# Performance work log

Hardware: AMD Instinct MI355X
Metric: run time of the kernel (lower is better)

The kernel has to match this reference:

```python
import jax, jax.numpy as jnp
import numpy as np

B, N, D, L, NREPEAT = 32, 577, 384, 12, 4
H = 4 * D  # mlp hidden
EPS = 1e-6


def ln(x, w, b):
    mu = jnp.mean(x, axis=-1, keepdims=True)
    var = jnp.mean(jnp.square(x - mu), axis=-1, keepdims=True)
    return (x - mu) * jax.lax.rsqrt(var + EPS) * w + b


def setup_inputs() -> dict:
    key = jax.random.key(0)
    ks = jax.random.split(key, 16)
    s = 0.02
    return {
        "x": jax.random.normal(ks[0], (B, N, D), dtype=jnp.float32),
        "norm1_w": jnp.ones((L, D), jnp.float32),
        "norm1_b": jnp.zeros((L, D), jnp.float32),
        "qkv_w": jax.random.normal(ks[1], (L, 3 * D, D), jnp.float32) * s,
        "qkv_b": jnp.zeros((L, 3 * D), jnp.float32),
        "qn_w": jnp.ones((L, D), jnp.float32),
        "qn_b": jnp.zeros((L, D), jnp.float32),
        "kn_w": jnp.ones((L, D), jnp.float32),
        "kn_b": jnp.zeros((L, D), jnp.float32),
        "an_w": jnp.ones((L, D), jnp.float32),
        "an_b": jnp.zeros((L, D), jnp.float32),
        "proj_w": jax.random.normal(ks[2], (L, D, D), jnp.float32) * s,
        "proj_b": jnp.zeros((L, D), jnp.float32),
        "ls1": jnp.full((L, D), 1e-5, jnp.float32),
        "norm2_w": jnp.ones((L, D), jnp.float32),
        "norm2_b": jnp.zeros((L, D), jnp.float32),
        "fc1_w": jax.random.normal(ks[3], (L, H, D), jnp.float32) * s,
        "fc1_b": jnp.zeros((L, H), jnp.float32),
        "fc2_w": jax.random.normal(ks[4], (L, D, H), jnp.float32) * s,
        "fc2_b": jnp.zeros((L, D), jnp.float32),
        "ls2": jnp.full((L, D), 1e-5, jnp.float32),
    }


def _forward(x, norm1_w, norm1_b, qkv_w, qkv_b, qn_w, qn_b, kn_w, kn_b,
             an_w, an_b, proj_w, proj_b, ls1, norm2_w, norm2_b,
             fc1_w, fc1_b, fc2_w, fc2_b, ls2):
    scale = 1.0 / np.sqrt(D).astype(np.float32)
    x_prime = x
    history = []  # list of [B, 1, D] cls tokens, grows each repeat
    for _ in range(NREPEAT):
        new_cls = x[:, 0:1]
        x = jnp.concatenate([new_cls, x_prime[:, 1:]], axis=1)  # [B, N, D]
        mem = jnp.concatenate([x] + history, axis=1)            # [B, N+t, D]
        for l in range(L):
            res1 = x
            xn = ln(x, norm1_w[l], norm1_b[l])
            # manual qkv split: q from normed x, k/v from UNNORMED mem
            q = xn @ qkv_w[l, :D].T + qkv_b[l, :D]
            k = mem @ qkv_w[l, D:2 * D].T + qkv_b[l, D:2 * D]
            v = mem @ qkv_w[l, 2 * D:].T + qkv_b[l, 2 * D:]
            q = ln(q, qn_w[l], qn_b[l])
            k = ln(k, kn_w[l], kn_b[l])
            # single-head SDPA over full width D
            attn = jax.nn.softmax(jnp.einsum('bqd,bkd->bqk', q, k) * scale, axis=-1)
            prod = jnp.einsum('bqk,bkd->bqd', attn, v)
            prod = ln(prod, an_w[l], an_b[l])
            proj = prod @ proj_w[l].T + proj_b[l]
            x = proj * ls1[l] + res1
            res2 = x
            x2 = ln(x, norm2_w[l], norm2_b[l])
            h = jax.nn.gelu(x2 @ fc1_w[l].T + fc1_b[l], approximate=False)
            x1 = h @ fc2_w[l].T + fc2_b[l]
            x = x1 * ls2[l] + res2
        history.append(new_cls)
    return x


def reference(x, norm1_w, norm1_b, qkv_w, qkv_b, qn_w, qn_b, kn_w, kn_b,
              an_w, an_b, proj_w, proj_b, ls1, norm2_w, norm2_b,
              fc1_w, fc1_b, fc2_w, fc2_b, ls2):
    return _forward(x, norm1_w, norm1_b, qkv_w, qkv_b, qn_w, qn_b, kn_w, kn_b,
                    an_w, an_b, proj_w, proj_b, ls1, norm2_w, norm2_b,
                    fc1_w, fc1_b, fc2_w, fc2_b, ls2)
```

## Files before the change

### kernel.cpp

```cpp
#include <hip/hip_runtime.h>
#include <math.h>

#define BB 32
#define NN 577
#define DD 384
#define HD 1536
#define LL 12
#define MP 640
#define NRPT 4

typedef __attribute__((ext_vector_type(8))) short bf16x8;
typedef __attribute__((ext_vector_type(4))) float f32x4;

__device__ __forceinline__ unsigned short f2bf(float f){
  unsigned u = __builtin_bit_cast(unsigned, f);
  u += 0x7fffu + ((u >> 16) & 1u);
  return (unsigned short)(u >> 16);
}
__device__ __forceinline__ float bf2f(unsigned short s){
  unsigned u = ((unsigned)s) << 16;
  return __builtin_bit_cast(float, u);
}

__device__ __forceinline__ void async16(void* lds, const void* g){
  __builtin_amdgcn_global_load_lds(
      (const __attribute__((address_space(1))) unsigned int*)g,
      (__attribute__((address_space(3))) unsigned int*)lds, 16, 0, 0);
}

__global__ void prep_k(float* __restrict__ x, const float* __restrict__ xp,
                       float* __restrict__ cls_r, const float* __restrict__ cls_hist,
                       unsigned short* __restrict__ mem, int r){
  int i = blockIdx.x * 256 + threadIdx.x;
  if (i >= BB*MP*DD) return;
  int d = i % DD;
  int n = (i / DD) % MP;
  int b = i / (MP*DD);
  float v; bool wr = true;
  if (n == 0){ v = x[(size_t)b*NN*DD + d]; cls_r[b*DD + d] = v; }
  else if (n < NN){ v = xp[((size_t)b*NN + n)*DD + d]; x[((size_t)b*NN + n)*DD + d] = v; wr = (r==0); }
  else if (n < NN + r){ v = cls_hist[(size_t)(n-NN)*BB*DD + b*DD + d]; wr = (n == NN + r - 1); }
  else { v = 0.f; wr = (r==0); }
  if (wr) mem[i] = f2bf(v);
}

__global__ void cast_all_k(const float* __restrict__ qkvw, const float* __restrict__ pw,
                           const float* __restrict__ f1w, const float* __restrict__ f2w,
                           unsigned short* __restrict__ wbuf){
  int i = blockIdx.x * 256 + threadIdx.x;
  const int QKV = 3*DD*DD;
  const int PRJ = DD*DD;
  const int F1  = HD*DD;
  const int TOT = QKV + PRJ + 2*F1;
  if (i >= LL*TOT) return;
  int l = i / TOT, j = i % TOT;
  float v;
  if (j < QKV) v = qkvw[(size_t)l*QKV + j];
  else if (j < QKV+PRJ) v = pw[(size_t)l*PRJ + (j-QKV)];
  else if (j < QKV+PRJ+F1) v = f1w[(size_t)l*F1 + (j-QKV-PRJ)];
  else v = f2w[(size_t)l*F1 + (j-QKV-PRJ-F1)];
  wbuf[i] = f2bf(v);
}

template<typename T>
__global__ __launch_bounds__(256) void ln4_k(const T* __restrict__ in, const float* __restrict__ w,
                                             const float* __restrict__ bias, unsigned short* __restrict__ out,
                                             int nrows){
  int row = blockIdx.x*4 + (threadIdx.x >> 6);
  if (row >= nrows) return;
  int lane = threadIdx.x & 63;
  const T* p = in + (size_t)row*DD;
  float v[6];
  if constexpr (sizeof(T) == 4){
    const float* pf = (const float*)p;
    float4 a = *(const float4*)(pf + lane*4);
    float2 c = *(const float2*)(pf + 256 + lane*2);
    v[0]=a.x; v[1]=a.y; v[2]=a.z; v[3]=a.w; v[4]=c.x; v[5]=c.y;
  } else {
    const unsigned short* ps = (const unsigned short*)p;
    ushort4 a = *(const ushort4*)(ps + lane*4);
    ushort2 c = *(const ushort2*)(ps + 256 + lane*2);
    v[0]=bf2f(a.x); v[1]=bf2f(a.y); v[2]=bf2f(a.z); v[3]=bf2f(a.w);
    v[4]=bf2f(c.x); v[5]=bf2f(c.y);
  }
  float s = v[0]+v[1]+v[2]+v[3]+v[4]+v[5];
  #pragma unroll
  for (int o=32;o;o>>=1) s += __shfl_xor(s, o, 64);
  float mu = s * (1.f/DD);
  float q = 0.f;
  #pragma unroll
  for (int i=0;i<6;i++){ float t = v[i]-mu; q += t*t; }
  #pragma unroll
  for (int o=32;o;o>>=1) q += __shfl_xor(q, o, 64);
  float rs = rsqrtf(q*(1.f/DD) + 1e-6f);
  float4 w4 = *(const float4*)(w + lane*4);
  float2 w2 = *(const float2*)(w + 256 + lane*2);
  float4 b4 = *(const float4*)(bias + lane*4);
  float2 b2 = *(const float2*)(bias + 256 + lane*2);
  unsigned short* po = out + (size_t)row*DD;
  ushort4 o4;
  o4.x = f2bf((v[0]-mu)*rs*w4.x + b4.x);
  o4.y = f2bf((v[1]-mu)*rs*w4.y + b4.y);
  o4.z = f2bf((v[2]-mu)*rs*w4.z + b4.z);
  o4.w = f2bf((v[3]-mu)*rs*w4.w + b4.w);
  *(ushort4*)(po + lane*4) = o4;
  ushort2 o2;
  o2.x = f2bf((v[4]-mu)*rs*w2.x + b2.x);
  o2.y = f2bf((v[5]-mu)*rs*w2.y + b2.y);
  *(ushort2*)(po + 256 + lane*2) = o2;
}

__global__ __launch_bounds__(256) void fixup_k(
    const unsigned short* __restrict__ mem,
    const unsigned short* __restrict__ wq,
    const float* __restrict__ qkvb,
    const float* __restrict__ knw, const float* __restrict__ knb,
    unsigned short* __restrict__ kc,
    unsigned short* __restrict__ vc,
    int row2){
  int task = blockIdx.x*4 + (threadIdx.x >> 6);
  int lane = threadIdx.x & 63;
  int kind = task & 1;
  int rsel = (task >> 1) & 1;
  int b    = task >> 2;
  int row  = rsel ? row2 : 0;
  const unsigned short* mrow = mem + ((size_t)b*MP + row)*DD;
  const unsigned short* W = wq + (size_t)(kind+1)*DD*DD;
  const float* bias = qkvb + (kind+1)*DD;

  float acc[6] = {0,0,0,0,0,0};
  for (int i=0;i<48;i++){
    bf16x8 m8 = *(const bf16x8*)(mrow + i*8);
    float mf[8];
    #pragma unroll
    for (int j=0;j<8;j++) mf[j] = bf2f((unsigned short)m8[j]);
    #pragma unroll
    for (int c=0;c<6;c++){
      bf16x8 w8 = *(const bf16x8*)(W + (size_t)(lane + c*64)*DD + i*8);
      #pragma unroll
      for (int j=0;j<8;j++) acc[c] += mf[j]*bf2f((unsigned short)w8[j]);
    }
  }
  #pragma unroll
  for (int c=0;c<6;c++) acc[c] += bias[lane + c*64];

  if (kind == 0){
    float s1 = 0.f, s2 = 0.f;
    #pragma unroll
    for (int c=0;c<6;c++){ s1 += acc[c]; s2 += acc[c]*acc[c]; }
    #pragma unroll
    for (int o=32;o;o>>=1){ s1 += __shfl_xor(s1, o, 64); s2 += __shfl_xor(s2, o, 64); }
    float mu = s1*(1.f/DD);
    float var = s2*(1.f/DD) - mu*mu;
    float rs = rsqrtf(fmaxf(var, 0.f) + 1e-6f);
    unsigned short* out = kc + ((size_t)b*MP + row)*DD;
    #pragma unroll
    for (int c=0;c<6;c++){
      int col = lane + c*64;
      out[col] = f2bf((acc[c]-mu)*rs*knw[col] + knb[col]);
    }
  } else {
    #pragma unroll
    for (int c=0;c<6;c++){
      int d = lane + c*64;
      vc[((size_t)b*DD + d)*MP + row] = f2bf(acc[c]);
    }
  }
}

__device__ __forceinline__ void gemm_body(
    unsigned short (*a_sh)[128*32], unsigned short (*b_sh)[128*32],
    const unsigned short* __restrict__ Ab, int lda, int arows,
    const unsigned short* __restrict__ Bb, int ldb, int brows,
    const float* __restrict__ bias, int K, int N,
    unsigned short* __restrict__ oB, int ldo, int orows,
    int epi, int row0, int col0){

  int tid  = threadIdx.x;
  int wave = tid >> 6, lane = tid & 63;
  int lr = lane & 15, kg = lane >> 4;
  int wm = wave >> 1, wn = wave & 1;

  f32x4 zf = {0.f,0.f,0.f,0.f};
  f32x4 acc[4][4];
  #pragma unroll
  for (int i=0;i<4;i++)
    #pragma unroll
    for (int j=0;j<4;j++) acc[i][j] = zf;

  int ra[2], rb[2], kc[2];
  #pragma unroll
  for (int it=0; it<2; it++){
    int c = tid + it*256;
    int r = row0 + (c>>2); if (r > arows-1) r = arows-1;
    ra[it] = r;
    r = col0 + (c>>2); if (r > brows-1) r = brows-1;
    rb[it] = r;
    kc[it] = (c&3)*8;
  }

  for (int k0 = 0; k0 < K; k0 += 64){
    #pragma unroll
    for (int p=0;p<2;p++){
      #pragma unroll
      for (int it=0; it<2; it++){
        async16(&a_sh[p][(it*256 + wave*64)*8], Ab + (size_t)ra[it]*lda + k0 + p*32 + kc[it]);
        async16(&b_sh[p][(it*256 + wave*64)*8], Bb + (size_t)rb[it]*ldb + k0 + p*32 + kc[it]);
      }
    }
    __syncthreads();
    #pragma unroll
    for (int p=0;p<2;p++){
      bf16x8 af[4], bfr[4];
      #pragma unroll
      for (int i=0;i<4;i++){
        af[i]  = *(const bf16x8*)&a_sh[p][(wm*64 + i*16 + lr)*32 + kg*8];
        bfr[i] = *(const bf16x8*)&b_sh[p][(wn*64 + i*16 + lr)*32 + kg*8];
      }
      #pragma unroll
      for (int i=0;i<4;i++)
        #pragma unroll
        for (int j=0;j<4;j++)
          acc[i][j] = __builtin_amdgcn_mfma_f32_16x16x32_bf16(af[i], bfr[j], acc[i][j], 0,0,0);
    }
    __syncthreads();
  }

  #pragma unroll
  for (int mi=0;mi<4;mi++)
    #pragma unroll
    for (int ni=0;ni<4;ni++)
      #pragma unroll
      for (int r=0;r<4;r++){
        int row = row0 + wm*64 + mi*16 + kg*4 + r;
        int col = col0 + wn*64 + ni*16 + lr;
        if (row >= orows || col >= N) continue;
        float vv = acc[mi][ni][r];
        vv += (epi == 0) ? bias[col] : bias[row];
        oB[(size_t)row*ldo + col] = f2bf(vv);
      }
}

__global__ __launch_bounds__(256) void gemmqkv_k(
    const unsigned short* __restrict__ xn, const unsigned short* __restrict__ mem,
    const unsigned short* __restrict__ wq, const float* __restrict__ qkvb,
    unsigned short* __restrict__ qout, unsigned short* __restrict__ kout,
    unsigned short* __restrict__ vout, int QR){

  __shared__ unsigned short a_sh[2][128*32];
  __shared__ unsigned short b_sh[2][128*32];

  int bid = blockIdx.x;
  const unsigned short *A, *B;
  const float* bias;
  unsigned short* out;
  int arows, brows, N, ldo, orows, epi, row0, col0;

  if (bid < 435){
    int gx = bid % 3, gy = bid / 3;
    A = xn; arows = QR; B = wq; brows = 384;
    bias = qkvb; N = 384; out = qout; ldo = 384; orows = QR; epi = 0;
    row0 = gy*128; col0 = gx*128;
  } else if (bid < 915){
    int t = bid - 435; int gx = t % 3, gy = t / 3;
    A = mem; arows = BB*MP; B = wq + DD*DD; brows = 384;
    bias = qkvb + DD; N = 384; out = kout; ldo = 384; orows = BB*MP; epi = 0;
    row0 = gy*128; col0 = gx*128;
  } else {
    int t = bid - 915; int z = t/15; int rem = t%15; int gx = rem % 5, gy = rem / 5;
    A = wq + 2*DD*DD; arows = 384;
    B = mem + (size_t)z*MP*DD; brows = MP;
    bias = qkvb + 2*DD; N = MP; out = vout + (size_t)z*DD*MP; ldo = MP; orows = 384; epi = 1;
    row0 = gy*128; col0 = gx*128;
  }
  gemm_body(a_sh, b_sh, A, 384, arows, B, 384, brows, bias, 384, N, out, ldo, orows, epi, row0, col0);
}

template<int EPI>
__global__ __launch_bounds__(256) void gemm128(
    const unsigned short* __restrict__ A, int lda, int arows, long sA,
    const unsigned short* __restrict__ B, int ldb, int brows, long sB,
    const float* __restrict__ bias,
    int K, int N,
    float* __restrict__ outF, unsigned short* __restrict__ outB,
    int ldo, int orows, long sO,
    const float* __restrict__ ls){

  __shared__ unsigned short a_sh[2][128*32];
  __shared__ unsigned short b_sh[2][128*32];

  int tid  = threadIdx.x;
  int wave = tid >> 6, lane = tid & 63;
  int lr = lane & 15, kg = lane >> 4;
  int wm = wave >> 1, wn = wave & 1;
  int z = blockIdx.z;
  int row0 = blockIdx.y * 128;
  int col0 = blockIdx.x * 128;

  const unsigned short* Ab = A + (size_t)z*sA;
  const unsigned short* Bb = B + (size_t)z*sB;

  f32x4 zf = {0.f,0.f,0.f,0.f};
  f32x4 acc[4][4];
  #pragma unroll
  for (int i=0;i<4;i++)
    #pragma unroll
    for (int j=0;j<4;j++) acc[i][j] = zf;

  int ra[2], rb[2], kc[2];
  #pragma unroll
  for (int it=0; it<2; it++){
    int c = tid + it*256;
    int r = row0 + (c>>2); if (r > arows-1) r = arows-1;
    ra[it] = r;
    r = col0 + (c>>2); if (r > brows-1) r = brows-1;
    rb[it] = r;
    kc[it] = (c&3)*8;
  }

  for (int k0 = 0; k0 < K; k0 += 64){
    #pragma unroll
    for (int p=0;p<2;p++){
      #pragma unroll
      for (int it=0; it<2; it++){
        unsigned short* la = &a_sh[p][(it*256 + wave*64)*8];
        unsigned short* lb = &b_sh[p][(it*256 + wave*64)*8];
        async16(la, Ab + (size_t)ra[it]*lda + k0 + p*32 + kc[it]);
        async16(lb, Bb + (size_t)rb[it]*ldb + k0 + p*32 + kc[it]);
      }
    }
    __syncthreads();
    #pragma unroll
    for (int p=0;p<2;p++){
      bf16x8 af[4], bfr[4];
      #pragma unroll
      for (int i=0;i<4;i++){
        af[i]  = *(const bf16x8*)&a_sh[p][(wm*64 + i*16 + lr)*32 + kg*8];
        bfr[i] = *(const bf16x8*)&b_sh[p][(wn*64 + i*16 + lr)*32 + kg*8];
      }
      #pragma unroll
      for (int i=0;i<4;i++)
        #pragma unroll
        for (int j=0;j<4;j++)
          acc[i][j] = __builtin_amdgcn_mfma_f32_16x16x32_bf16(af[i], bfr[j], acc[i][j], 0,0,0);
    }
    __syncthreads();
  }

  float* oF = outF ? outF + (size_t)z*sO : nullptr;
  unsigned short* oB = outB ? outB + (size_t)z*sO : nullptr;

  #pragma unroll
  for (int mi=0;mi<4;mi++)
    #pragma unroll
    for (int ni=0;ni<4;ni++)
      #pragma unroll
      for (int r=0;r<4;r++){
        int row = row0 + wm*64 + mi*16 + kg*4 + r;
        int col = col0 + wn*64 + ni*16 + lr;
        if (row >= orows || col >= N) continue;
        float vv = acc[mi][ni][r];
        size_t idx = (size_t)row*ldo + col;
        if (EPI == 0){
          if (bias) vv += bias[col];
          oB[idx] = f2bf(vv);
        } else if (EPI == 1){
          vv += bias[row];
          oB[idx] = f2bf(vv);
        } else if (EPI == 2){
          vv += bias[col];
          oF[idx] = vv*ls[col] + oF[idx];
        } else {
          vv += bias[col];
          float g = 0.5f*vv*(1.f + erff(vv*0.70710678118f));
          oB[idx] = f2bf(g);
        }
      }
}

__global__ __launch_bounds__(256, 2) void attn_k(
    const unsigned short* __restrict__ qraw,
    const float* __restrict__ qw, const float* __restrict__ qb_,
    const unsigned short* __restrict__ kb,
    const unsigned short* __restrict__ vT,
    const float* __restrict__ anw, const float* __restrict__ anb,
    unsigned short* __restrict__ out, int M){

  __shared__ unsigned short k_sh[32*384];
  __shared__ unsigned short v_sh[384*32];
  __shared__ unsigned short p_sh[64*56];

  int tid = threadIdx.x;
  int wv = tid >> 6, lane = tid & 63;
  int lr = lane & 15, kg = lane >> 4;
  int b = blockIdx.y, qt0 = blockIdx.x * 64;

  bf16x8 qf[12];
  {
    int qrow = qt0 + wv*16 + lr; if (qrow > NN-1) qrow = NN-1;
    const unsigned short* qp = qraw + ((size_t)b*NN + qrow)*DD;
    float s1 = 0.f, s2 = 0.f;
    #pragma unroll
    for (int ks=0; ks<12; ks++){
      qf[ks] = *(const bf16x8*)(qp + ks*32 + kg*8);
      #pragma unroll
      for (int j=0;j<8;j++){
        float t = bf2f((unsigned short)qf[ks][j]);
        s1 += t; s2 += t*t;
      }
    }
    s1 += __shfl_xor(s1, 16, 64); s1 += __shfl_xor(s1, 32, 64);
    s2 += __shfl_xor(s2, 16, 64); s2 += __shfl_xor(s2, 32, 64);
    const float SC = 0.05103103588f;
    float mu = s1 * (1.f/DD);
    float var = s2 * (1.f/DD) - mu*mu;
    float rs = rsqrtf(fmaxf(var, 0.f) + 1e-6f) * SC;
    #pragma unroll
    for (int ks=0; ks<12; ks++){
      int c0 = ks*32 + kg*8;
      float4 wa = *(const float4*)(qw + c0);
      float4 wb = *(const float4*)(qw + c0 + 4);
      float4 ba = *(const float4*)(qb_ + c0);
      float4 bb = *(const float4*)(qb_ + c0 + 4);
      bf16x8 t;
      t[0] = (short)f2bf((bf2f((unsigned short)qf[ks][0])-mu)*rs*wa.x + ba.x*SC);
      t[1] = (short)f2bf((bf2f((unsigned short)qf[ks][1])-mu)*rs*wa.y + ba.y*SC);
      t[2] = (short)f2bf((bf2f((unsigned short)qf[ks][2])-mu)*rs*wa.z + ba.z*SC);
      t[3] = (short)f2bf((bf2f((unsigned short)qf[ks][3])-mu)*rs*wa.w + ba.w*SC);
      t[4] = (short)f2bf((bf2f((unsigned short)qf[ks][4])-mu)*rs*wb.x + bb.x*SC);
      t[5] = (short)f2bf((bf2f((unsigned short)qf[ks][5])-mu)*rs*wb.y + bb.y*SC);
      t[6] = (short)f2bf((bf2f((unsigned short)qf[ks][6])-mu)*rs*wb.z + bb.z*SC);
      t[7] = (short)f2bf((bf2f((unsigned short)qf[ks][7])-mu)*rs*wb.w + bb.w*SC);
      qf[ks] = t;
    }
  }

  f32x4 zf = {0.f,0.f,0.f,0.f};
  f32x4 O[24];
  #pragma unroll
  for (int i=0;i<24;i++) O[i] = zf;
  float m_run[4], l_run[4];
  #pragma unroll
  for (int r=0;r<4;r++){ m_run[r] = -INFINITY; l_run[r] = 0.f; }

  for (int kt=0; kt<19; kt++){
    __syncthreads();
    #pragma unroll
    for (int i=0;i<6;i++){
      int L = i*256 + tid;
      int row = L/48, c = L%48;
      int gc = (c & ~7) | ((c ^ row) & 7);
      async16(&k_sh[L*8], kb + ((size_t)b*MP + kt*32 + row)*DD + gc*8);
    }
    #pragma unroll
    for (int i=0;i<6;i++){
      int L = i*256 + tid;
      int row = L>>2;
      int gc = (L&3) ^ (row&3);
      async16(&v_sh[L*8], vT + ((size_t)b*DD + row)*MP + kt*32 + gc*8);
    }
    __syncthreads();

    f32x4 s[2] = {zf, zf};
    __builtin_amdgcn_s_setprio(1);
    #pragma unroll
    for (int ks=0; ks<12; ks++){
      int c = ks*4 + kg;
      #pragma unroll
      for (int nk=0; nk<2; nk++){
        int krow = nk*16 + lr;
        bf16x8 bk = *(const bf16x8*)&k_sh[krow*DD + ((c & ~7) | ((c ^ krow)&7))*8];
        s[nk] = __builtin_amdgcn_mfma_f32_16x16x32_bf16(qf[ks], bk, s[nk], 0,0,0);
      }
    }
    __builtin_amdgcn_s_setprio(0);
    #pragma unroll
    for (int nk=0; nk<2; nk++){
      if (kt*32 + nk*16 + lr >= M){
        s[nk][0] = -INFINITY; s[nk][1] = -INFINITY; s[nk][2] = -INFINITY; s[nk][3] = -INFINITY;
      }
    }
    float vmax[4];
    #pragma unroll
    for (int r=0;r<4;r++){
      float v = fmaxf(s[0][r], s[1][r]);
      v = fmaxf(v, __shfl_xor(v, 1, 64));
      v = fmaxf(v, __shfl_xor(v, 2, 64));
      v = fmaxf(v, __shfl_xor(v, 4, 64));
      v = fmaxf(v, __shfl_xor(v, 8, 64));
      vmax[r] = v;
    }
    bool small = (vmax[0] <= m_run[0] + 8.f) & (vmax[1] <= m_run[1] + 8.f)
               & (vmax[2] <= m_run[2] + 8.f) & (vmax[3] <= m_run[3] + 8.f);
    if (!__all(small)){
      #pragma unroll
      for (int r=0;r<4;r++){
        float mn = fmaxf(m_run[r], vmax[r]);
        float al = __expf(m_run[r] - mn);
        m_run[r] = mn;
        l_run[r] *= al;
        #pragma unroll
        for (int ni=0;ni<24;ni++) O[ni][r] *= al;
      }
    }
    #pragma unroll
    for (int nk=0;nk<2;nk++)
      #pragma unroll
      for (int r=0;r<4;r++)
        s[nk][r] = __expf(s[nk][r] - m_run[r]);
    #pragma unroll
    for (int r=0;r<4;r++){
      float v = s[0][r] + s[1][r];
      v += __shfl_xor(v, 1, 64);
      v += __shfl_xor(v, 2, 64);
      v += __shfl_xor(v, 4, 64);
      v += __shfl_xor(v, 8, 64);
      l_run[r] += v;
    }
    #pragma unroll
    for (int nk=0;nk<2;nk++)
      #pragma unroll
      for (int r=0;r<4;r++)
        p_sh[(wv*16 + kg*4 + r)*56 + nk*16 + lr] = f2bf(s[nk][r]);
    __syncthreads();

    bf16x8 ap = *(const bf16x8*)&p_sh[(wv*16 + lr)*56 + kg*8];
    __builtin_amdgcn_s_setprio(1);
    #pragma unroll
    for (int ni=0;ni<24;ni++){
      int d = ni*16 + lr;
      bf16x8 bv = *(const bf16x8*)&v_sh[d*32 + ((kg ^ (d&3))*8)];
      O[ni] = __builtin_amdgcn_mfma_f32_16x16x32_bf16(ap, bv, O[ni], 0,0,0);
    }
    __builtin_amdgcn_s_setprio(0);
  }

  float inv[4];
  #pragma unroll
  for (int r=0;r<4;r++) inv[r] = 1.f / l_run[r];
  float s1[4] = {0,0,0,0}, s2[4] = {0,0,0,0};
  #pragma unroll
  for (int ni=0;ni<24;ni++)
    #pragma unroll
    for (int r=0;r<4;r++){
      float x = O[ni][r]*inv[r];
      O[ni][r] = x;
      s1[r] += x; s2[r] += x*x;
    }
  #pragma unroll
  for (int r=0;r<4;r++){
    #pragma unroll
    for (int o=1;o<16;o<<=1){ s1[r] += __shfl_xor(s1[r], o, 64); s2[r] += __shfl_xor(s2[r], o, 64); }
  }
  float mu[4], rs[4];
  #pragma unroll
  for (int r=0;r<4;r++){
    mu[r] = s1[r]*(1.f/DD);
    float var = s2[r]*(1.f/DD) - mu[r]*mu[r];
    rs[r] = rsqrtf(fmaxf(var, 0.f) + 1e-6f);
  }
  int rowb = qt0 + wv*16 + kg*4;
  #pragma unroll
  for (int ni=0;ni<24;ni++){
    int col = ni*16 + lr;
    float wc = anw[col], bc = anb[col];
    #pragma unroll
    for (int r=0;r<4;r++){
      int qrow = rowb + r;
      if (qrow < NN)
        out[((size_t)b*NN + qrow)*DD + col] = f2bf((O[ni][r]-mu[r])*rs[r]*wc + bc);
    }
  }
}


extern "C" void kernel_launch(void* const* d_in, const int* in_sizes, int n_in,
                              void* d_out, int out_size, void* d_ws, size_t ws_size,
                              hipStream_t stream){
  const float* x_in = (const float*)d_in[0];
  const float* n1w  = (const float*)d_in[1];
  const float* n1b  = (const float*)d_in[2];
  const float* qkvw = (const float*)d_in[3];
  const float* qkvb = (const float*)d_in[4];
  const float* qnw  = (const float*)d_in[5];
  const float* qnb  = (const float*)d_in[6];
  const float* knw  = (const float*)d_in[7];
  const float* knb  = (const float*)d_in[8];
  const float* anw  = (const float*)d_in[9];
  const float* anb  = (const float*)d_in[10];
  const float* pw   = (const float*)d_in[11];
  const float* pb   = (const float*)d_in[12];
  const float* ls1  = (const float*)d_in[13];
  const float* n2w  = (const float*)d_in[14];
  const float* n2b  = (const float*)d_in[15];
  const float* f1w  = (const float*)d_in[16];
  const float* f1b  = (const float*)d_in[17];
  const float* f2w  = (const float*)d_in[18];
  const float* f2bb = (const float*)d_in[19];
  const float* ls2  = (const float*)d_in[20];

  char* ws = (char*)d_ws;
  size_t off = 0;
  auto alloc = [&](size_t bytes)->char* {
    char* p = ws + off;
    off = (off + bytes + 255) & ~(size_t)255;
    return p;
  };

  const int QKV = 3*DD*DD, PRJ = DD*DD, F1 = HD*DD;
  const size_t WTOT = (size_t)QKV + PRJ + 2*F1;
  const size_t SLOT = (size_t)BB*MP*DD;

  unsigned short* wbuf  = (unsigned short*)alloc((size_t)LL*WTOT*2);
  float*          cls_h = (float*)         alloc((size_t)NRPT*BB*DD*4);
  unsigned short* mem_bf= (unsigned short*)alloc(SLOT*2);
  unsigned short* pool  = (unsigned short*)alloc(6*SLOT*2);
  unsigned short* kcache = (unsigned short*)alloc((size_t)LL*SLOT*2);
  unsigned short* vcache = (unsigned short*)alloc((size_t)LL*SLOT*2);
  bool use_cache = (off <= ws_size);

  unsigned short* S0 = pool;
  unsigned short* S1 = pool + SLOT;
  unsigned short* S2 = pool + 2*SLOT;
  unsigned short* S3 = pool + 3*SLOT;
  unsigned short* S5 = pool + 5*SLOT;

  unsigned short* xn    = S0;
  unsigned short* qraw  = S1;
  unsigned short* prodn = S3;
  unsigned short* x2    = S0;
  unsigned short* h     = S1;

  float* xf = (float*)d_out;

  auto cg = [](size_t n){ return dim3((unsigned)((n + 255) / 256)); };

  hipMemcpyAsync(xf, x_in, (size_t)BB*NN*DD*4, hipMemcpyDeviceToDevice, stream);

  const int RT  = (BB*NN + 127)/128;
  const int QR  = BB*NN;
  const int KR  = BB*MP;

  cast_all_k<<<cg((size_t)LL*WTOT),256,0,stream>>>(qkvw, pw, f1w, f2w, wbuf);

  for (int r = 0; r < NRPT; r++){
    int M = NN + r;
    prep_k<<<cg((size_t)BB*MP*DD),256,0,stream>>>(xf, x_in, cls_h + (size_t)r*BB*DD, cls_h, mem_bf, r);
    for (int l = 0; l < LL; l++){
      const unsigned short* wl = wbuf + (size_t)l*WTOT;
      const unsigned short* wq = wl;
      const unsigned short* wp = wl + QKV;
      const unsigned short* w1 = wl + QKV + PRJ;
      const unsigned short* w2 = wl + QKV + PRJ + F1;

      bool cached = use_cache;
      unsigned short* kbuf = cached ? kcache + (size_t)l*SLOT : S2;
      unsigned short* vbuf = cached ? vcache + (size_t)l*SLOT : S5;

      ln4_k<float><<<cg((size_t)QR*64),256,0,stream>>>(xf, n1w + l*DD, n1b + l*DD, xn, QR);

      if (!cached || r == 0){
        gemmqkv_k<<<1395,256,0,stream>>>(xn, mem_bf, wq, qkvb + l*3*DD, qraw, kbuf, vbuf, QR);
        ln4_k<unsigned short><<<cg((size_t)KR*64),256,0,stream>>>(kbuf, knw + l*DD, knb + l*DD, kbuf, KR);
      } else {
        gemm128<0><<<dim3(3,RT,1),256,0,stream>>>(xn,384,QR,0, wq,384,384,0,
            qkvb + l*3*DD, 384,384, nullptr,qraw,384,QR,0, nullptr);
        fixup_k<<<32,256,0,stream>>>(mem_bf, wq, qkvb + l*3*DD,
                                     knw + l*DD, knb + l*DD, kbuf, vbuf, NN + r - 1);
      }

      attn_k<<<dim3(10,BB),256,0,stream>>>(qraw, qnw + l*DD, qnb + l*DD, kbuf, vbuf,
                                           anw + l*DD, anb + l*DD, prodn, M);
      gemm128<2><<<dim3(3,RT,1),256,0,stream>>>(prodn,384,QR,0, wp,384,384,0,
          pb + l*DD, 384,384, xf,nullptr,384,QR,0, ls1 + l*DD);
      ln4_k<float><<<cg((size_t)QR*64),256,0,stream>>>(xf, n2w + l*DD, n2b + l*DD, x2, QR);
      gemm128<3><<<dim3(HD/128,RT,1),256,0,stream>>>(x2,384,QR,0, w1,384,HD,0,
          f1b + l*HD, 384,HD, nullptr,h,HD,QR,0, nullptr);
      gemm128<2><<<dim3(3,RT,1),256,0,stream>>>(h,HD,QR,0, w2,HD,384,0,
          f2bb + l*DD, HD,384, xf,nullptr,384,QR,0, ls2 + l*DD);
    }
  }
}
```

Baseline: 15.62 ms.

## Batch K/V projection and K-norm across all layers into single launches

```diff
diff --git a/kernel.cpp b/kernel.cpp
--- a/kernel.cpp
+++ b/kernel.cpp
@@ -110,23 +110,68 @@
   *(ushort2*)(po + 256 + lane*2) = o2;
 }
 
-__global__ __launch_bounds__(256) void fixup_k(
+__global__ __launch_bounds__(256) void kln_all_k(
+    unsigned short* __restrict__ kbase, long kstride,
+    const float* __restrict__ knw, const float* __restrict__ knb, int l0){
+  const int RPL4 = (BB*MP)/4;
+  int li = blockIdx.x / RPL4;
+  int row = (blockIdx.x % RPL4)*4 + (threadIdx.x >> 6);
+  int lane = threadIdx.x & 63;
+  unsigned short* p = kbase + (size_t)li*kstride + (size_t)row*DD;
+  const float* w = knw + (size_t)(l0+li)*DD;
+  const float* bias = knb + (size_t)(l0+li)*DD;
+  float v[6];
+  ushort4 a = *(const ushort4*)(p + lane*4);
+  ushort2 c = *(const ushort2*)(p + 256 + lane*2);
+  v[0]=bf2f(a.x); v[1]=bf2f(a.y); v[2]=bf2f(a.z); v[3]=bf2f(a.w);
+  v[4]=bf2f(c.x); v[5]=bf2f(c.y);
+  float s = v[0]+v[1]+v[2]+v[3]+v[4]+v[5];
+  #pragma unroll
+  for (int o=32;o;o>>=1) s += __shfl_xor(s, o, 64);
+  float mu = s * (1.f/DD);
+  float q = 0.f;
+  #pragma unroll
+  for (int i=0;i<6;i++){ float t = v[i]-mu; q += t*t; }
+  #pragma unroll
+  for (int o=32;o;o>>=1) q += __shfl_xor(q, o, 64);
+  float rs = rsqrtf(q*(1.f/DD) + 1e-6f);
+  float4 w4 = *(const float4*)(w + lane*4);
+  float2 w2 = *(const float2*)(w + 256 + lane*2);
+  float4 b4 = *(const float4*)(bias + lane*4);
+  float2 b2 = *(const float2*)(bias + 256 + lane*2);
+  ushort4 o4;
+  o4.x = f2bf((v[0]-mu)*rs*w4.x + b4.x);
+  o4.y = f2bf((v[1]-mu)*rs*w4.y + b4.y);
+  o4.z = f2bf((v[2]-mu)*rs*w4.z + b4.z);
+  o4.w = f2bf((v[3]-mu)*rs*w4.w + b4.w);
+  *(ushort4*)(p + lane*4) = o4;
+  ushort2 o2;
+  o2.x = f2bf((v[4]-mu)*rs*w2.x + b2.x);
+  o2.y = f2bf((v[5]-mu)*rs*w2.y + b2.y);
+  *(ushort2*)(p + 256 + lane*2) = o2;
+}
+
+__global__ __launch_bounds__(256) void fixup_all_k(
     const unsigned short* __restrict__ mem,
-    const unsigned short* __restrict__ wq,
+    const unsigned short* __restrict__ wbuf,
     const float* __restrict__ qkvb,
-    const float* __restrict__ knw, const float* __restrict__ knb,
-    unsigned short* __restrict__ kc,
-    unsigned short* __restrict__ vc,
+    const float* __restrict__ knw_, const float* __restrict__ knb_,
+    unsigned short* __restrict__ kcache,
+    unsigned short* __restrict__ vcache,
     int row2){
-  int task = blockIdx.x*4 + (threadIdx.x >> 6);
+  const int QKV = 3*DD*DD, PRJ = DD*DD, F1 = HD*DD;
+  const size_t WTOT = (size_t)QKV + PRJ + 2*F1;
+  const size_t SLOT = (size_t)BB*MP*DD;
+  int l    = blockIdx.x >> 5;
+  int task = (blockIdx.x & 31)*4 + (threadIdx.x >> 6);
   int lane = threadIdx.x & 63;
   int kind = task & 1;
   int rsel = (task >> 1) & 1;
   int b    = task >> 2;
   int row  = rsel ? row2 : 0;
   const unsigned short* mrow = mem + ((size_t)b*MP + row)*DD;
-  const unsigned short* W = wq + (size_t)(kind+1)*DD*DD;
-  const float* bias = qkvb + (kind+1)*DD;
+  const unsigned short* W = wbuf + (size_t)l*WTOT + (size_t)(kind+1)*DD*DD;
+  const float* bias = qkvb + (size_t)l*3*DD + (kind+1)*DD;
 
   float acc[6] = {0,0,0,0,0,0};
   for (int i=0;i<48;i++){
@@ -153,13 +198,16 @@
     float mu = s1*(1.f/DD);
     float var = s2*(1.f/DD) - mu*mu;
     float rs = rsqrtf(fmaxf(var, 0.f) + 1e-6f);
-    unsigned short* out = kc + ((size_t)b*MP + row)*DD;
+    const float* knw = knw_ + (size_t)l*DD;
+    const float* knb = knb_ + (size_t)l*DD;
+    unsigned short* out = kcache + (size_t)l*SLOT + ((size_t)b*MP + row)*DD;
     #pragma unroll
     for (int c=0;c<6;c++){
       int col = lane + c*64;
       out[col] = f2bf((acc[c]-mu)*rs*knw[col] + knb[col]);
     }
   } else {
+    unsigned short* vc = vcache + (size_t)l*SLOT;
     #pragma unroll
     for (int c=0;c<6;c++){
       int d = lane + c*64;
@@ -241,6 +289,35 @@
       }
 }
 
+__global__ __launch_bounds__(256) void kv_mega_k(
+    const unsigned short* __restrict__ mem,
+    const unsigned short* __restrict__ wbuf,
+    const float* __restrict__ qkvb,
+    unsigned short* __restrict__ kbase, long kstride,
+    unsigned short* __restrict__ vbase, long vstride,
+    int l0){
+  __shared__ unsigned short a_sh[2][128*32];
+  __shared__ unsigned short b_sh[2][128*32];
+  const int QKV = 3*DD*DD, PRJ = DD*DD, F1 = HD*DD;
+  const size_t WTOT = (size_t)QKV + PRJ + 2*F1;
+
+  int li = blockIdx.x / 960;
+  int t  = blockIdx.x % 960;
+  int l  = l0 + li;
+  const unsigned short* wl = wbuf + (size_t)l*WTOT;
+  const float* bl = qkvb + (size_t)l*3*DD;
+
+  if (t < 480){
+    int gx = t % 3, gy = t / 3;
+    gemm_body(a_sh, b_sh, mem, 384, BB*MP, wl + DD*DD, 384, 384, bl + DD,
+              384, 384, kbase + (size_t)li*kstride, 384, BB*MP, 0, gy*128, gx*128);
+  } else {
+    int u = t - 480; int z = u/15; int rem = u%15; int gx = rem % 5, gy = rem / 5;
+    gemm_body(a_sh, b_sh, wl + 2*DD*DD, 384, 384, mem + (size_t)z*MP*DD, 384, MP, bl + 2*DD,
+              384, MP, vbase + (size_t)li*vstride + (size_t)z*DD*MP, MP, 384, 1, gy*128, gx*128);
+  }
+}
+
 __global__ __launch_bounds__(256) void gemmqkv_k(
     const unsigned short* __restrict__ xn, const unsigned short* __restrict__ mem,
     const unsigned short* __restrict__ wq, const float* __restrict__ qkvb,
@@ -251,29 +328,19 @@
   __shared__ unsigned short b_sh[2][128*32];
 
   int bid = blockIdx.x;
-  const unsigned short *A, *B;
-  const float* bias;
-  unsigned short* out;
-  int arows, brows, N, ldo, orows, epi, row0, col0;
-
   if (bid < 435){
     int gx = bid % 3, gy = bid / 3;
-    A = xn; arows = QR; B = wq; brows = 384;
-    bias = qkvb; N = 384; out = qout; ldo = 384; orows = QR; epi = 0;
-    row0 = gy*128; col0 = gx*128;
+    gemm_body(a_sh, b_sh, xn, 384, QR, wq, 384, 384, qkvb, 384, 384,
+              qout, 384, QR, 0, gy*128, gx*128);
   } else if (bid < 915){
     int t = bid - 435; int gx = t % 3, gy = t / 3;
-    A = mem; arows = BB*MP; B = wq + DD*DD; brows = 384;
-    bias = qkvb + DD; N = 384; out = kout; ldo = 384; orows = BB*MP; epi = 0;
-    row0 = gy*128; col0 = gx*128;
+    gemm_body(a_sh, b_sh, mem, 384, BB*MP, wq + DD*DD, 384, 384, qkvb + DD,
+              384, 384, kout, 384, BB*MP, 0, gy*128, gx*128);
   } else {
     int t = bid - 915; int z = t/15; int rem = t%15; int gx = rem % 5, gy = rem / 5;
-    A = wq + 2*DD*DD; arows = 384;
-    B = mem + (size_t)z*MP*DD; brows = MP;
-    bias = qkvb + 2*DD; N = MP; out = vout + (size_t)z*DD*MP; ldo = MP; orows = 384; epi = 1;
-    row0 = gy*128; col0 = gx*128;
-  }
-  gemm_body(a_sh, b_sh, A, 384, arows, B, 384, brows, bias, 384, N, out, ldo, orows, epi, row0, col0);
+    gemm_body(a_sh, b_sh, wq + 2*DD*DD, 384, 384, mem + (size_t)z*MP*DD, 384, MP, qkvb + 2*DD,
+              384, MP, vout + (size_t)z*DD*MP, MP, 384, 1, gy*128, gx*128);
+  }
 }
 
 template<int EPI>
@@ -599,37 +666,50 @@
   const float* f2bb = (const float*)d_in[19];
   const float* ls2  = (const float*)d_in[20];
 
+  const int QKV = 3*DD*DD, PRJ = DD*DD, F1 = HD*DD;
+  const size_t WTOT = (size_t)QKV + PRJ + 2*F1;
+  const size_t SLOT = (size_t)BB*MP*DD;
+  const size_t SLB  = SLOT*2;
+
   char* ws = (char*)d_ws;
   size_t off = 0;
-  auto alloc = [&](size_t bytes)->char* {
+  auto take = [&](size_t bytes)->char* {
     char* p = ws + off;
     off = (off + bytes + 255) & ~(size_t)255;
     return p;
   };
 
-  const int QKV = 3*DD*DD, PRJ = DD*DD, F1 = HD*DD;
-  const size_t WTOT = (size_t)QKV + PRJ + 2*F1;
-  const size_t SLOT = (size_t)BB*MP*DD;
-
-  unsigned short* wbuf  = (unsigned short*)alloc((size_t)LL*WTOT*2);
-  float*          cls_h = (float*)         alloc((size_t)NRPT*BB*DD*4);
-  unsigned short* mem_bf= (unsigned short*)alloc(SLOT*2);
-  unsigned short* pool  = (unsigned short*)alloc(6*SLOT*2);
-  unsigned short* kcache = (unsigned short*)alloc((size_t)LL*SLOT*2);
-  unsigned short* vcache = (unsigned short*)alloc((size_t)LL*SLOT*2);
-  bool use_cache = (off <= ws_size);
-
-  unsigned short* S0 = pool;
-  unsigned short* S1 = pool + SLOT;
-  unsigned short* S2 = pool + 2*SLOT;
-  unsigned short* S3 = pool + 3*SLOT;
-  unsigned short* S5 = pool + 5*SLOT;
+  unsigned short* wbuf   = (unsigned short*)take((size_t)LL*WTOT*2);
+  float*          cls_h  = (float*)         take((size_t)NRPT*BB*DD*4);
+  unsigned short* mem_bf = (unsigned short*)take(SLB);
+  unsigned short* S0     = (unsigned short*)take(SLB);
+  unsigned short* S3     = (unsigned short*)take(SLB);
+  unsigned short* HQ     = (unsigned short*)take(4*SLB);
+
+  bool fullcache = (off + 2*(size_t)LL*SLB <= ws_size);
+  int G = 0;
+  unsigned short *kvk = nullptr, *kvv = nullptr;
+  long kstr = 0, vstr = 0;
+  if (fullcache){
+    kvk = (unsigned short*)take((size_t)LL*SLB);
+    kvv = (unsigned short*)take((size_t)LL*SLB);
+    kstr = (long)SLOT; vstr = (long)SLOT;
+    G = LL;
+  } else {
+    size_t avail = (ws_size > off) ? ws_size - off : 0;
+    G = (int)(avail / (2*SLB)); if (G > LL) G = LL; if (G < 0) G = 0;
+    if (G > 0){
+      kvk = (unsigned short*)take((size_t)G*2*SLB);
+      kvv = kvk + SLOT;
+      kstr = (long)(2*SLOT); vstr = (long)(2*SLOT);
+    }
+  }
 
   unsigned short* xn    = S0;
-  unsigned short* qraw  = S1;
+  unsigned short* x2    = S0;
   unsigned short* prodn = S3;
-  unsigned short* x2    = S0;
-  unsigned short* h     = S1;
+  unsigned short* qraw  = HQ;
+  unsigned short* h     = HQ;
 
   float* xf = (float*)d_out;
 
@@ -646,29 +726,16 @@
   for (int r = 0; r < NRPT; r++){
     int M = NN + r;
     prep_k<<<cg((size_t)BB*MP*DD),256,0,stream>>>(xf, x_in, cls_h + (size_t)r*BB*DD, cls_h, mem_bf, r);
-    for (int l = 0; l < LL; l++){
+
+    auto chain7 = [&](int l, unsigned short* kbuf, unsigned short* vbuf){
       const unsigned short* wl = wbuf + (size_t)l*WTOT;
       const unsigned short* wq = wl;
       const unsigned short* wp = wl + QKV;
       const unsigned short* w1 = wl + QKV + PRJ;
       const unsigned short* w2 = wl + QKV + PRJ + F1;
-
-      bool cached = use_cache;
-      unsigned short* kbuf = cached ? kcache + (size_t)l*SLOT : S2;
-      unsigned short* vbuf = cached ? vcache + (size_t)l*SLOT : S5;
-
       ln4_k<float><<<cg((size_t)QR*64),256,0,stream>>>(xf, n1w + l*DD, n1b + l*DD, xn, QR);
-
-      if (!cached || r == 0){
-        gemmqkv_k<<<1395,256,0,stream>>>(xn, mem_bf, wq, qkvb + l*3*DD, qraw, kbuf, vbuf, QR);
-        ln4_k<unsigned short><<<cg((size_t)KR*64),256,0,stream>>>(kbuf, knw + l*DD, knb + l*DD, kbuf, KR);
-      } else {
-        gemm128<0><<<dim3(3,RT,1),256,0,stream>>>(xn,384,QR,0, wq,384,384,0,
-            qkvb + l*3*DD, 384,384, nullptr,qraw,384,QR,0, nullptr);
-        fixup_k<<<32,256,0,stream>>>(mem_bf, wq, qkvb + l*3*DD,
-                                     knw + l*DD, knb + l*DD, kbuf, vbuf, NN + r - 1);
-      }
-
+      gemm128<0><<<dim3(3,RT,1),256,0,stream>>>(xn,384,QR,0, wq,384,384,0,
+          qkvb + l*3*DD, 384,384, nullptr,qraw,384,QR,0, nullptr);
       attn_k<<<dim3(10,BB),256,0,stream>>>(qraw, qnw + l*DD, qnb + l*DD, kbuf, vbuf,
                                            anw + l*DD, anb + l*DD, prodn, M);
       gemm128<2><<<dim3(3,RT,1),256,0,stream>>>(prodn,384,QR,0, wp,384,384,0,
@@ -678,6 +745,47 @@
           f1b + l*HD, 384,HD, nullptr,h,HD,QR,0, nullptr);
       gemm128<2><<<dim3(3,RT,1),256,0,stream>>>(h,HD,QR,0, w2,HD,384,0,
           f2bb + l*DD, HD,384, xf,nullptr,384,QR,0, ls2 + l*DD);
-    }
-  }
-}
+    };
+
+    if (fullcache){
+      if (r == 0){
+        kv_mega_k<<<LL*960,256,0,stream>>>(mem_bf, wbuf, qkvb, kvk, kstr, kvv, vstr, 0);
+        kln_all_k<<<LL*(KR/4),256,0,stream>>>(kvk, kstr, knw, knb, 0);
+      } else {
+        fixup_all_k<<<LL*32,256,0,stream>>>(mem_bf, wbuf, qkvb, knw, knb, kvk, kvv, NN + r - 1);
+      }
+      for (int l = 0; l < LL; l++)
+        chain7(l, kvk + (size_t)l*kstr, kvv + (size_t)l*vstr);
+    } else if (G > 0){
+      for (int g0 = 0; g0 < LL; g0 += G){
+        int gc = (g0 + G <= LL) ? G : (LL - g0);
+        kv_mega_k<<<gc*960,256,0,stream>>>(mem_bf, wbuf, qkvb, kvk, kstr, kvv, vstr, g0);
+        kln_all_k<<<gc*(KR/4),256,0,stream>>>(kvk, kstr, knw, knb, g0);
+        for (int l = g0; l < g0 + gc; l++)
+          chain7(l, kvk + (size_t)(l-g0)*kstr, kvv + (size_t)(l-g0)*vstr);
+      }
+    } else {
+      for (int l = 0; l < LL; l++){
+        const unsigned short* wl = wbuf + (size_t)l*WTOT;
+        const unsigned short* wq = wl;
+        const unsigned short* wp = wl + QKV;
+        const unsigned short* w1 = wl + QKV + PRJ;
+        const unsigned short* w2 = wl + QKV + PRJ + F1;
+        unsigned short* kbuf = S3;
+        unsigned short* vbuf = HQ + 2*SLOT;
+        ln4_k<float><<<cg((size_t)QR*64),256,0,stream>>>(xf, n1w + l*DD, n1b + l*DD, xn, QR);
+        gemmqkv_k<<<1395,256,0,stream>>>(xn, mem_bf, wq, qkvb + l*3*DD, qraw, kbuf, vbuf, QR);
+        kln_all_k<<<(KR/4),256,0,stream>>>(kbuf, 0, knw + l*DD, knb + l*DD, 0);
+        attn_k<<<dim3(10,BB),256,0,stream>>>(qraw, qnw + l*DD, qnb + l*DD, kbuf, vbuf,
+                                             anw + l*DD, anb + l*DD, prodn, M);
+        gemm128<2><<<dim3(3,RT,1),256,0,stream>>>(prodn,384,QR,0, wp,384,384,0,
+            pb + l*DD, 384,384, xf,nullptr,384,QR,0, ls1 + l*DD);
+        ln4_k<float><<<cg((size_t)QR*64),256,0,stream>>>(xf, n2w + l*DD, n2b + l*DD, x2, QR);
+        gemm128<3><<<dim3(HD/128,RT,1),256,0,stream>>>(x2,384,QR,0, w1,384,HD,0,
+            f1b + l*HD, 384,HD, nullptr,h,HD,QR,0, nullptr);
+        gemm128<2><<<dim3(3,RT,1),256,0,stream>>>(h,HD,QR,0, w2,HD,384,0,
+            f2bb + l*DD, HD,384, xf,nullptr,384,QR,0, ls2 + l*DD);
+      }
+    }
+  }
+}
```

New measurement: 15.66 ms. About the same (+0.3%).

## Drop cross-repeat K/V cache and fuse key LayerNorm into attention tile loads

Applied to the files above, without the earlier changes.

```diff
diff --git a/kernel.cpp b/kernel.cpp
--- a/kernel.cpp
+++ b/kernel.cpp
@@ -62,27 +62,17 @@
   wbuf[i] = f2bf(v);
 }
 
-template<typename T>
-__global__ __launch_bounds__(256) void ln4_k(const T* __restrict__ in, const float* __restrict__ w,
+__global__ __launch_bounds__(256) void ln4_k(const float* __restrict__ in, const float* __restrict__ w,
                                              const float* __restrict__ bias, unsigned short* __restrict__ out,
                                              int nrows){
   int row = blockIdx.x*4 + (threadIdx.x >> 6);
   if (row >= nrows) return;
   int lane = threadIdx.x & 63;
-  const T* p = in + (size_t)row*DD;
+  const float* pf = in + (size_t)row*DD;
   float v[6];
-  if constexpr (sizeof(T) == 4){
-    const float* pf = (const float*)p;
-    float4 a = *(const float4*)(pf + lane*4);
-    float2 c = *(const float2*)(pf + 256 + lane*2);
-    v[0]=a.x; v[1]=a.y; v[2]=a.z; v[3]=a.w; v[4]=c.x; v[5]=c.y;
-  } else {
-    const unsigned short* ps = (const unsigned short*)p;
-    ushort4 a = *(const ushort4*)(ps + lane*4);
-    ushort2 c = *(const ushort2*)(ps + 256 + lane*2);
-    v[0]=bf2f(a.x); v[1]=bf2f(a.y); v[2]=bf2f(a.z); v[3]=bf2f(a.w);
-    v[4]=bf2f(c.x); v[5]=bf2f(c.y);
-  }
+  float4 a = *(const float4*)(pf + lane*4);
+  float2 c = *(const float2*)(pf + 256 + lane*2);
+  v[0]=a.x; v[1]=a.y; v[2]=a.z; v[3]=a.w; v[4]=c.x; v[5]=c.y;
   float s = v[0]+v[1]+v[2]+v[3]+v[4]+v[5];
   #pragma unroll
   for (int o=32;o;o>>=1) s += __shfl_xor(s, o, 64);
@@ -110,64 +100,6 @@
   *(ushort2*)(po + 256 + lane*2) = o2;
 }
 
-__global__ __launch_bounds__(256) void fixup_k(
-    const unsigned short* __restrict__ mem,
-    const unsigned short* __restrict__ wq,
-    const float* __restrict__ qkvb,
-    const float* __restrict__ knw, const float* __restrict__ knb,
-    unsigned short* __restrict__ kc,
-    unsigned short* __restrict__ vc,
-    int row2){
-  int task = blockIdx.x*4 + (threadIdx.x >> 6);
-  int lane = threadIdx.x & 63;
-  int kind = task & 1;
-  int rsel = (task >> 1) & 1;
-  int b    = task >> 2;
-  int row  = rsel ? row2 : 0;
-  const unsigned short* mrow = mem + ((size_t)b*MP + row)*DD;
-  const unsigned short* W = wq + (size_t)(kind+1)*DD*DD;
-  const float* bias = qkvb + (kind+1)*DD;
-
-  float acc[6] = {0,0,0,0,0,0};
-  for (int i=0;i<48;i++){
-    bf16x8 m8 = *(const bf16x8*)(mrow + i*8);
-    float mf[8];
-    #pragma unroll
-    for (int j=0;j<8;j++) mf[j] = bf2f((unsigned short)m8[j]);
-    #pragma unroll
-    for (int c=0;c<6;c++){
-      bf16x8 w8 = *(const bf16x8*)(W + (size_t)(lane + c*64)*DD + i*8);
-      #pragma unroll
-      for (int j=0;j<8;j++) acc[c] += mf[j]*bf2f((unsigned short)w8[j]);
-    }
-  }
-  #pragma unroll
-  for (int c=0;c<6;c++) acc[c] += bias[lane + c*64];
-
-  if (kind == 0){
-    float s1 = 0.f, s2 = 0.f;
-    #pragma unroll
-    for (int c=0;c<6;c++){ s1 += acc[c]; s2 += acc[c]*acc[c]; }
-    #pragma unroll
-    for (int o=32;o;o>>=1){ s1 += __shfl_xor(s1, o, 64); s2 += __shfl_xor(s2, o, 64); }
-    float mu = s1*(1.f/DD);
-    float var = s2*(1.f/DD) - mu*mu;
-    float rs = rsqrtf(fmaxf(var, 0.f) + 1e-6f);
-    unsigned short* out = kc + ((size_t)b*MP + row)*DD;
-    #pragma unroll
-    for (int c=0;c<6;c++){
-      int col = lane + c*64;
-      out[col] = f2bf((acc[c]-mu)*rs*knw[col] + knb[col]);
-    }
-  } else {
-    #pragma unroll
-    for (int c=0;c<6;c++){
-      int d = lane + c*64;
-      vc[((size_t)b*DD + d)*MP + row] = f2bf(acc[c]);
-    }
-  }
-}
-
 __device__ __forceinline__ void gemm_body(
     unsigned short (*a_sh)[128*32], unsigned short (*b_sh)[128*32],
     const unsigned short* __restrict__ Ab, int lda, int arows,
@@ -251,29 +183,19 @@
   __shared__ unsigned short b_sh[2][128*32];
 
   int bid = blockIdx.x;
-  const unsigned short *A, *B;
-  const float* bias;
-  unsigned short* out;
-  int arows, brows, N, ldo, orows, epi, row0, col0;
-
   if (bid < 435){
     int gx = bid % 3, gy = bid / 3;
-    A = xn; arows = QR; B = wq; brows = 384;
-    bias = qkvb; N = 384; out = qout; ldo = 384; orows = QR; epi = 0;
-    row0 = gy*128; col0 = gx*128;
+    gemm_body(a_sh, b_sh, xn, 384, QR, wq, 384, 384, qkvb, 384, 384,
+              qout, 384, QR, 0, gy*128, gx*128);
   } else if (bid < 915){
     int t = bid - 435; int gx = t % 3, gy = t / 3;
-    A = mem; arows = BB*MP; B = wq + DD*DD; brows = 384;
-    bias = qkvb + DD; N = 384; out = kout; ldo = 384; orows = BB*MP; epi = 0;
-    row0 = gy*128; col0 = gx*128;
+    gemm_body(a_sh, b_sh, mem, 384, BB*MP, wq + DD*DD, 384, 384, qkvb + DD,
+              384, 384, kout, 384, BB*MP, 0, gy*128, gx*128);
   } else {
     int t = bid - 915; int z = t/15; int rem = t%15; int gx = rem % 5, gy = rem / 5;
-    A = wq + 2*DD*DD; arows = 384;
-    B = mem + (size_t)z*MP*DD; brows = MP;
-    bias = qkvb + 2*DD; N = MP; out = vout + (size_t)z*DD*MP; ldo = MP; orows = 384; epi = 1;
-    row0 = gy*128; col0 = gx*128;
-  }
-  gemm_body(a_sh, b_sh, A, 384, arows, B, 384, brows, bias, 384, N, out, ldo, orows, epi, row0, col0);
+    gemm_body(a_sh, b_sh, wq + 2*DD*DD, 384, 384, mem + (size_t)z*MP*DD, 384, MP, qkvb + 2*DD,
+              384, MP, vout + (size_t)z*DD*MP, MP, 384, 1, gy*128, gx*128);
+  }
 }
 
 template<int EPI>
@@ -361,13 +283,7 @@
         if (row >= orows || col >= N) continue;
         float vv = acc[mi][ni][r];
         size_t idx = (size_t)row*ldo + col;
-        if (EPI == 0){
-          if (bias) vv += bias[col];
-          oB[idx] = f2bf(vv);
-        } else if (EPI == 1){
-          vv += bias[row];
-          oB[idx] = f2bf(vv);
-        } else if (EPI == 2){
+        if (EPI == 2){
           vv += bias[col];
           oF[idx] = vv*ls[col] + oF[idx];
         } else {
@@ -381,7 +297,8 @@
 __global__ __launch_bounds__(256, 2) void attn_k(
     const unsigned short* __restrict__ qraw,
     const float* __restrict__ qw, const float* __restrict__ qb_,
-    const unsigned short* __restrict__ kb,
+    const unsigned short* __restrict__ kraw,
+    const float* __restrict__ knw, const float* __restrict__ knb,
     const unsigned short* __restrict__ vT,
     const float* __restrict__ anw, const float* __restrict__ anb,
     unsigned short* __restrict__ out, int M){
@@ -450,7 +367,7 @@
       int L = i*256 + tid;
       int row = L/48, c = L%48;
       int gc = (c & ~7) | ((c ^ row) & 7);
-      async16(&k_sh[L*8], kb + ((size_t)b*MP + kt*32 + row)*DD + gc*8);
+      async16(&k_sh[L*8], kraw + ((size_t)b*MP + kt*32 + row)*DD + gc*8);
     }
     #pragma unroll
     for (int i=0;i<6;i++){
@@ -458,6 +375,45 @@
       int row = L>>2;
       int gc = (L&3) ^ (row&3);
       async16(&v_sh[L*8], vT + ((size_t)b*DD + row)*MP + kt*32 + gc*8);
+    }
+    __syncthreads();
+
+    {
+      int row8 = tid >> 3;
+      int sub  = tid & 7;
+      unsigned short* kr = &k_sh[row8*384];
+      float s1 = 0.f, s2 = 0.f;
+      #pragma unroll
+      for (int c6=0;c6<6;c6++){
+        bf16x8 v8 = *(const bf16x8*)&kr[(sub*6 + c6)*8];
+        #pragma unroll
+        for (int j=0;j<8;j++){ float t = bf2f((unsigned short)v8[j]); s1 += t; s2 += t*t; }
+      }
+      s1 += __shfl_xor(s1, 1, 64); s1 += __shfl_xor(s1, 2, 64); s1 += __shfl_xor(s1, 4, 64);
+      s2 += __shfl_xor(s2, 1, 64); s2 += __shfl_xor(s2, 2, 64); s2 += __shfl_xor(s2, 4, 64);
+      float mu = s1 * (1.f/DD);
+      float var = s2 * (1.f/DD) - mu*mu;
+      float rs = rsqrtf(fmaxf(var, 0.f) + 1e-6f);
+      #pragma unroll
+      for (int c6=0;c6<6;c6++){
+        int cpos = sub*6 + c6;
+        int gc = (cpos & ~7) | ((cpos ^ row8) & 7);
+        bf16x8 v8 = *(const bf16x8*)&kr[cpos*8];
+        float4 wa = *(const float4*)(knw + gc*8);
+        float4 wb = *(const float4*)(knw + gc*8 + 4);
+        float4 ba = *(const float4*)(knb + gc*8);
+        float4 bb = *(const float4*)(knb + gc*8 + 4);
+        bf16x8 o;
+        o[0] = (short)f2bf((bf2f((unsigned short)v8[0])-mu)*rs*wa.x + ba.x);
+        o[1] = (short)f2bf((bf2f((unsigned short)v8[1])-mu)*rs*wa.y + ba.y);
+        o[2] = (short)f2bf((bf2f((unsigned short)v8[2])-mu)*rs*wa.z + ba.z);
+        o[3] = (short)f2bf((bf2f((unsigned short)v8[3])-mu)*rs*wa.w + ba.w);
+        o[4] = (short)f2bf((bf2f((unsigned short)v8[4])-mu)*rs*wb.x + bb.x);
+        o[5] = (short)f2bf((bf2f((unsigned short)v8[5])-mu)*rs*wb.y + bb.y);
+        o[6] = (short)f2bf((bf2f((unsigned short)v8[6])-mu)*rs*wb.z + bb.z);
+        o[7] = (short)f2bf((bf2f((unsigned short)v8[7])-mu)*rs*wb.w + bb.w);
+        *(bf16x8*)&kr[cpos*8] = o;
+      }
     }
     __syncthreads();
 
@@ -599,37 +555,33 @@
   const float* f2bb = (const float*)d_in[19];
   const float* ls2  = (const float*)d_in[20];
 
+  const int QKV = 3*DD*DD, PRJ = DD*DD, F1 = HD*DD;
+  const size_t WTOT = (size_t)QKV + PRJ + 2*F1;
+  const size_t SLOT = (size_t)BB*MP*DD;
+  const size_t SLB  = SLOT*2;
+
   char* ws = (char*)d_ws;
   size_t off = 0;
-  auto alloc = [&](size_t bytes)->char* {
+  auto take = [&](size_t bytes)->char* {
     char* p = ws + off;
     off = (off + bytes + 255) & ~(size_t)255;
     return p;
   };
 
-  const int QKV = 3*DD*DD, PRJ = DD*DD, F1 = HD*DD;
-  const size_t WTOT = (size_t)QKV + PRJ + 2*F1;
-  const size_t SLOT = (size_t)BB*MP*DD;
-
-  unsigned short* wbuf  = (unsigned short*)alloc((size_t)LL*WTOT*2);
-  float*          cls_h = (float*)         alloc((size_t)NRPT*BB*DD*4);
-  unsigned short* mem_bf= (unsigned short*)alloc(SLOT*2);
-  unsigned short* pool  = (unsigned short*)alloc(6*SLOT*2);
-  unsigned short* kcache = (unsigned short*)alloc((size_t)LL*SLOT*2);
-  unsigned short* vcache = (unsigned short*)alloc((size_t)LL*SLOT*2);
-  bool use_cache = (off <= ws_size);
-
-  unsigned short* S0 = pool;
-  unsigned short* S1 = pool + SLOT;
-  unsigned short* S2 = pool + 2*SLOT;
-  unsigned short* S3 = pool + 3*SLOT;
-  unsigned short* S5 = pool + 5*SLOT;
+  unsigned short* wbuf   = (unsigned short*)take((size_t)LL*WTOT*2);
+  float*          cls_h  = (float*)         take((size_t)NRPT*BB*DD*4);
+  unsigned short* mem_bf = (unsigned short*)take(SLB);
+  unsigned short* S0     = (unsigned short*)take(SLB);
+  unsigned short* S3     = (unsigned short*)take(SLB);
+  unsigned short* HQ     = (unsigned short*)take(4*SLB);
 
   unsigned short* xn    = S0;
-  unsigned short* qraw  = S1;
+  unsigned short* x2    = S0;
   unsigned short* prodn = S3;
-  unsigned short* x2    = S0;
-  unsigned short* h     = S1;
+  unsigned short* qraw  = HQ;
+  unsigned short* kraw  = HQ + SLOT;
+  unsigned short* vTb   = HQ + 2*SLOT;
+  unsigned short* h     = HQ;
 
   float* xf = (float*)d_out;
 
@@ -639,7 +591,6 @@
 
   const int RT  = (BB*NN + 127)/128;
   const int QR  = BB*NN;
-  const int KR  = BB*MP;
 
   cast_all_k<<<cg((size_t)LL*WTOT),256,0,stream>>>(qkvw, pw, f1w, f2w, wbuf);
 
@@ -653,27 +604,14 @@
       const unsigned short* w1 = wl + QKV + PRJ;
       const unsigned short* w2 = wl + QKV + PRJ + F1;
 
-      bool cached = use_cache;
-      unsigned short* kbuf = cached ? kcache + (size_t)l*SLOT : S2;
-      unsigned short* vbuf = cached ? vcache + (size_t)l*SLOT : S5;
-
-      ln4_k<float><<<cg((size_t)QR*64),256,0,stream>>>(xf, n1w + l*DD, n1b + l*DD, xn, QR);
-
-      if (!cached || r == 0){
-        gemmqkv_k<<<1395,256,0,stream>>>(xn, mem_bf, wq, qkvb + l*3*DD, qraw, kbuf, vbuf, QR);
-        ln4_k<unsigned short><<<cg((size_t)KR*64),256,0,stream>>>(kbuf, knw + l*DD, knb + l*DD, kbuf, KR);
-      } else {
-        gemm128<0><<<dim3(3,RT,1),256,0,stream>>>(xn,384,QR,0, wq,384,384,0,
-            qkvb + l*3*DD, 384,384, nullptr,qraw,384,QR,0, nullptr);
-        fixup_k<<<32,256,0,stream>>>(mem_bf, wq, qkvb + l*3*DD,
-                                     knw + l*DD, knb + l*DD, kbuf, vbuf, NN + r - 1);
-      }
-
-      attn_k<<<dim3(10,BB),256,0,stream>>>(qraw, qnw + l*DD, qnb + l*DD, kbuf, vbuf,
+      ln4_k<<<cg((size_t)QR*64),256,0,stream>>>(xf, n1w + l*DD, n1b + l*DD, xn, QR);
+      gemmqkv_k<<<1395,256,0,stream>>>(xn, mem_bf, wq, qkvb + l*3*DD, qraw, kraw, vTb, QR);
+      attn_k<<<dim3(10,BB),256,0,stream>>>(qraw, qnw + l*DD, qnb + l*DD,
+                                           kraw, knw + l*DD, knb + l*DD, vTb,
                                            anw + l*DD, anb + l*DD, prodn, M);
       gemm128<2><<<dim3(3,RT,1),256,0,stream>>>(prodn,384,QR,0, wp,384,384,0,
           pb + l*DD, 384,384, xf,nullptr,384,QR,0, ls1 + l*DD);
-      ln4_k<float><<<cg((size_t)QR*64),256,0,stream>>>(xf, n2w + l*DD, n2b + l*DD, x2, QR);
+      ln4_k<<<cg((size_t)QR*64),256,0,stream>>>(xf, n2w + l*DD, n2b + l*DD, x2, QR);
       gemm128<3><<<dim3(HD/128,RT,1),256,0,stream>>>(x2,384,QR,0, w1,384,HD,0,
           f1b + l*HD, 384,HD, nullptr,h,HD,QR,0, nullptr);
       gemm128<2><<<dim3(3,RT,1),256,0,stream>>>(h,HD,QR,0, w2,HD,384,0,
```

Result: slower. 21.38 ms (+36.9%).
